# Optimization experiments

Measured on AMD Instinct MI355X. Metric: run time of the kernel, lower is better.

The kernel has to match this reference:

```python
import jax, jax.numpy as jnp
import numpy as np

EPS = 1e-5

def bn(x, g, b):
    # training-mode BatchNorm2d: normalize over all axes except channel axis 1
    ax = (0,) + tuple(range(2, x.ndim))
    m = x.mean(ax, keepdims=True)
    v = x.var(ax, keepdims=True)
    sh = (1, -1) + (1,) * (x.ndim - 2)
    return (x - m) * jax.lax.rsqrt(v + EPS) * g.reshape(sh) + b.reshape(sh)

def setup_inputs():
    key = jax.random.key(0)
    ks = jax.random.split(key, 7)
    N, C, H, W, G = 2, 128, 128, 128, 8
    gp = C // G  # group_planes = 16
    f32 = jnp.float32
    x = jax.random.normal(ks[0], (N, C, H, W), f32)
    wq = jax.random.normal(ks[1], (C // 2, C), f32) * np.float32(np.sqrt(1.0 / (C * gp)))
    wk = jax.random.normal(ks[2], (C // 2, C), f32) * np.float32(np.sqrt(1.0 / C))
    wv = jax.random.normal(ks[3], (C, C), f32) * np.float32(np.sqrt(1.0 / C))
    q_rel = jax.random.normal(ks[4], (gp // 2, 2 * H - 1), f32) * np.float32(np.sqrt(2.0 / C))
    k_rel = jax.random.normal(ks[5], (gp // 2, 2 * H - 1), f32) * np.float32(np.sqrt(2.0 / C))
    v_rel = jax.random.normal(ks[6], (gp, 2 * H - 1), f32) * np.float32(np.sqrt(1.0 / C))
    d = dict(x=x, wq=wq, wk=wk, wv=wv, q_rel=q_rel, k_rel=k_rel, v_rel=v_rel)
    for name, ch in [("bnq", C // 2), ("bnk", C // 2), ("bnv", C), ("bnqk", G), ("bnqr", G), ("bnkr", G), ("bnsv", C), ("bnsve", C)]:
        d[name + "_g"] = jnp.ones((ch,), f32)
        d[name + "_b"] = jnp.zeros((ch,), f32)
    return d

def reference(x, wq, wk, wv, q_rel, k_rel, v_rel, bnq_g, bnq_b, bnk_g, bnk_b, bnv_g, bnv_b, bnqk_g, bnqk_b, bnqr_g, bnqr_b, bnkr_g, bnkr_b, bnsv_g, bnsv_b, bnsve_g, bnsve_b):
    N, C, H, W = x.shape
    G = 8
    gp = C // G
    # 1x1 conv == channel matmul
    q = bn(jnp.einsum('oc,bchw->bohw', wq, x), bnq_g, bnq_b)
    k = bn(jnp.einsum('oc,bchw->bohw', wk, x), bnk_g, bnk_b)
    v = bn(jnp.einsum('oc,bchw->bohw', wv, x), bnv_g, bnv_b)
    # relative embedding gather: emb[c, j, i] = rel[c, j - i + H - 1]
    idx = jnp.arange(H)[:, None] - jnp.arange(H)[None, :] + (H - 1)  # [H, H]
    q_emb = q_rel[:, idx]
    k_emb = k_rel[:, idx]
    v_emb = v_rel[:, idx]
    qg = q.reshape(N, G, gp // 2, H, W)
    kg = k.reshape(N, G, gp // 2, H, W)
    vg = v.reshape(N, G, gp, H, W)
    qr = jnp.einsum('bgciw,cij->bgijw', qg, q_emb)
    qr = bn(qr.reshape(N, G, H * H, W), bnqr_g, bnqr_b).reshape(N, G, H, H, W)
    kr = jnp.einsum('bgciw,cij->bgijw', kg, k_emb)
    kr = bn(kr.reshape(N, G, H * H, W), bnkr_g, bnkr_b).reshape(N, G, H, H, W)
    kr = kr.transpose(0, 1, 3, 2, 4)
    qk = jnp.einsum('bgciw,bgcjw->bgijw', qg, kg)
    qk = bn(qk.reshape(N, G, H * H, W), bnqk_g, bnqk_b).reshape(N, G, H, H, W)
    sim = jax.nn.softmax(qk + qr + kr, axis=3)  # [N, G, H(i), H(j), W]
    sv = jnp.einsum('bgijw,bgcjw->bgciw', sim, vg).reshape(N, C, H, W)
    sve = jnp.einsum('bgijw,cji->bgciw', sim, v_emb).reshape(N, C, H, W)
    return bn(sv, bnsv_g, bnsv_b) + bn(sve, bnsve_g, bnsve_b)
```

## Files before the change

### kernel.cpp

```cpp
#include <hip/hip_runtime.h>
#include <hip/hip_fp16.h>


#define HW 16384

__device__ __forceinline__ float warp_sum(float v) {
#pragma unroll
  for (int o = 32; o > 0; o >>= 1) v += __shfl_down(v, o);
  return v;
}

__global__ __launch_bounds__(256) void k_transpose(const float* __restrict__ in, float* __restrict__ out) {
  __shared__ float t[32][33];
  int plane = blockIdx.y;
  int th = (blockIdx.x >> 2) * 32;
  int tw = (blockIdx.x & 3) * 32;
  const float* p = in + (size_t)plane * HW;
  float* q = out + (size_t)plane * HW;
  int lx = threadIdx.x, ly = threadIdx.y;
#pragma unroll
  for (int r = ly; r < 32; r += 8) t[r][lx] = p[(th + r) * 128 + tw + lx];
  __syncthreads();
#pragma unroll
  for (int r = ly; r < 32; r += 8) q[(tw + r) * 128 + th + lx] = t[lx][r];
}

__global__ __launch_bounds__(256) void k_wT(const float* __restrict__ wq, const float* __restrict__ wk,
                                            const float* __restrict__ wv, float* __restrict__ WT) {
  int idx = blockIdx.x * 256 + threadIdx.x;
  int och = idx & 255, c = idx >> 8;
  const float* wrow = och < 64 ? wq + och * 128 : (och < 128 ? wk + (och - 64) * 128 : wv + (och - 128) * 128);
  WT[c * 256 + och] = wrow[c];
}

__global__ __launch_bounds__(256) void k_qkv(const float* __restrict__ xT, const float* __restrict__ WT,
                                             float* __restrict__ qkvT) {
  __shared__ float Xs[64][64];
  __shared__ float Ws[64][64];
  int pb = blockIdx.x * 64;
  int ob = blockIdx.y * 64;
  int b = blockIdx.z;
  const float* xb = xT + (size_t)b * (128 * HW);
  int tid = threadIdx.x;
  int tx = tid & 15, ty = tid >> 4;
  float acc[4][4] = {};
  for (int ks = 0; ks < 2; ++ks) {
    for (int idx = tid; idx < 4096; idx += 256) {
      int c = idx >> 6, p = idx & 63;
      Xs[c][p] = xb[(ks * 64 + c) * HW + pb + p];
    }
    for (int idx = tid; idx < 4096; idx += 256) {
      int c = idx >> 6, o = idx & 63;
      Ws[c][o] = WT[(ks * 64 + c) * 256 + ob + o];
    }
    __syncthreads();
#pragma unroll 8
    for (int kk = 0; kk < 64; ++kk) {
      float a0 = Ws[kk][ty * 4 + 0], a1 = Ws[kk][ty * 4 + 1], a2 = Ws[kk][ty * 4 + 2], a3 = Ws[kk][ty * 4 + 3];
      float4 bv = *reinterpret_cast<const float4*>(&Xs[kk][tx * 4]);
      acc[0][0] += a0 * bv.x; acc[0][1] += a0 * bv.y; acc[0][2] += a0 * bv.z; acc[0][3] += a0 * bv.w;
      acc[1][0] += a1 * bv.x; acc[1][1] += a1 * bv.y; acc[1][2] += a1 * bv.z; acc[1][3] += a1 * bv.w;
      acc[2][0] += a2 * bv.x; acc[2][1] += a2 * bv.y; acc[2][2] += a2 * bv.z; acc[2][3] += a2 * bv.w;
      acc[3][0] += a3 * bv.x; acc[3][1] += a3 * bv.y; acc[3][2] += a3 * bv.z; acc[3][3] += a3 * bv.w;
    }
    __syncthreads();
  }
#pragma unroll
  for (int r = 0; r < 4; ++r) {
    int row = ob + ty * 4 + r;
    float4 o4 = make_float4(acc[r][0], acc[r][1], acc[r][2], acc[r][3]);
    *reinterpret_cast<float4*>(&qkvT[(size_t)(b * 256 + row) * HW + pb + tx * 4]) = o4;
  }
}

__global__ __launch_bounds__(256) void k_qkv_stats(const float* __restrict__ qkvT, double* __restrict__ statsQKV) {
  __shared__ float r1[4], r2[4];
  int ch = blockIdx.x;
  float s = 0.f, s2 = 0.f;
  for (int b = 0; b < 2; ++b) {
    const float* p = qkvT + (size_t)(b * 256 + ch) * HW;
    for (int idx = threadIdx.x; idx < HW; idx += 256) { float v = p[idx]; s += v; s2 += v * v; }
  }
  s = warp_sum(s); s2 = warp_sum(s2);
  int wid = threadIdx.x >> 6;
  if ((threadIdx.x & 63) == 0) { r1[wid] = s; r2[wid] = s2; }
  __syncthreads();
  if (threadIdx.x == 0) {
    statsQKV[2 * ch]     = (double)(r1[0] + r1[1] + r1[2] + r1[3]);
    statsQKV[2 * ch + 1] = (double)(r2[0] + r2[1] + r2[2] + r2[3]);
  }
}

__global__ __launch_bounds__(128) void k_rel_tables(const float* __restrict__ q_rel, const float* __restrict__ k_rel,
                                                    float* __restrict__ tabs) {
  int tbl = blockIdx.x / 44, item = blockIdx.x % 44;
  const float* rel = tbl ? k_rel : q_rel;
  float* out = tabs + tbl * 5632;
  int i = threadIdx.x;
  float s = 0.f;
  if (item < 8) {
    const float* r = rel + item * 255 + i;
    for (int d = 0; d < 128; ++d) s += r[d];
  } else {
    int p = item - 8;
    int pp = p, c = 0;
    while (pp >= 8 - c) { pp -= 8 - c; ++c; }
    int c2 = c + pp;
    const float* ra = rel + c * 255 + i;
    const float* rb = rel + c2 * 255 + i;
    for (int d = 0; d < 128; ++d) s += ra[d] * rb[d];
  }
  out[item * 128 + i] = s;
}

__global__ __launch_bounds__(128) void k_qkr_stats(
    const float* __restrict__ qkvT, const double* __restrict__ statsQKV,
    const float* __restrict__ bnq_g, const float* __restrict__ bnq_b,
    const float* __restrict__ bnk_g, const float* __restrict__ bnk_b,
    const float* __restrict__ tabs, double* __restrict__ statsA) {
  __shared__ float red[92][2];
  int slice = blockIdx.x;
  int w = slice & 127, g = (slice >> 7) & 7, b = slice >> 10;
  int i = threadIdx.x;
  float qn[8], kn[8];
  const float* qbase = qkvT + (size_t)(b * 256 + g * 8) * HW + w * 128 + i;
  const float* kbase = qkvT + (size_t)(b * 256 + 64 + g * 8) * HW + w * 128 + i;
#pragma unroll
  for (int c = 0; c < 8; ++c) {
    {
      int och = g * 8 + c;
      double su = statsQKV[2 * och], sq = statsQKV[2 * och + 1];
      double mu = su * (1.0 / 32768.0);
      float var = (float)(sq * (1.0 / 32768.0) - mu * mu);
      float sc = bnq_g[och] * rsqrtf(var + 1e-5f);
      qn[c] = qbase[c * HW] * sc + (bnq_b[och] - (float)mu * sc);
    }
    {
      int gi = g * 8 + c, och = 64 + gi;
      double su = statsQKV[2 * och], sq = statsQKV[2 * och + 1];
      double mu = su * (1.0 / 32768.0);
      float var = (float)(sq * (1.0 / 32768.0) - mu * mu);
      float sc = bnk_g[gi] * rsqrtf(var + 1e-5f);
      kn[c] = kbase[c * HW] * sc + (bnk_b[gi] - (float)mu * sc);
    }
  }
  float vals[92];
  int n = 0;
#pragma unroll
  for (int c = 0; c < 8; ++c) vals[n++] = qn[c];
#pragma unroll
  for (int c = 0; c < 8; ++c) vals[n++] = kn[c];
#pragma unroll
  for (int c = 0; c < 8; ++c)
#pragma unroll
    for (int c2 = c; c2 < 8; ++c2) vals[n++] = qn[c] * qn[c2];
#pragma unroll
  for (int c = 0; c < 8; ++c)
#pragma unroll
    for (int c2 = c; c2 < 8; ++c2) vals[n++] = kn[c] * kn[c2];
  float sqr = 0.f, s2qr = 0.f, skr = 0.f, s2kr = 0.f;
#pragma unroll
  for (int c = 0; c < 8; ++c) {
    sqr += qn[c] * tabs[c * 128 + i];
    skr += kn[c] * tabs[5632 + c * 128 + i];
  }
  {
    int p = 0;
#pragma unroll
    for (int c = 0; c < 8; ++c)
#pragma unroll
      for (int c2 = c; c2 < 8; ++c2) {
        float f = (c == c2) ? 1.f : 2.f;
        s2qr += f * qn[c] * qn[c2] * tabs[1024 + p * 128 + i];
        s2kr += f * kn[c] * kn[c2] * tabs[5632 + 1024 + p * 128 + i];
        ++p;
      }
  }
  vals[88] = sqr; vals[89] = s2qr; vals[90] = skr; vals[91] = s2kr;
  int lane = i & 63, wid = i >> 6;
#pragma unroll
  for (int vv = 0; vv < 92; ++vv) {
    float r = warp_sum(vals[vv]);
    if (lane == 0) red[vv][wid] = r;
  }
  __syncthreads();
  if (i == 0) {
    float f[92];
#pragma unroll
    for (int vv = 0; vv < 92; ++vv) f[vv] = red[vv][0] + red[vv][1];
    float sS = 0.f, s2S = 0.f;
#pragma unroll
    for (int c = 0; c < 8; ++c) sS += f[c] * f[8 + c];
    {
      int p = 0;
#pragma unroll
      for (int c = 0; c < 8; ++c)
#pragma unroll
        for (int c2 = c; c2 < 8; ++c2) { float fm = (c == c2) ? 1.f : 2.f; s2S += fm * f[16 + p] * f[52 + p]; ++p; }
    }
    atomicAdd(&statsA[(0 * 8 + g) * 2 + 0], (double)sS);
    atomicAdd(&statsA[(0 * 8 + g) * 2 + 1], (double)s2S);
    atomicAdd(&statsA[(1 * 8 + g) * 2 + 0], (double)f[88]);
    atomicAdd(&statsA[(1 * 8 + g) * 2 + 1], (double)f[89]);
    atomicAdd(&statsA[(2 * 8 + g) * 2 + 0], (double)f[90]);
    atomicAdd(&statsA[(2 * 8 + g) * 2 + 1], (double)f[91]);
  }
}

__global__ __launch_bounds__(256) void k_relT(const float* __restrict__ q_rel, const float* __restrict__ k_rel,
                                              float* __restrict__ relT) {
  int idx = blockIdx.x * 256 + threadIdx.x;
  if (idx < 2040) {
    int d = idx >> 3, c = idx & 7;
    relT[idx] = q_rel[c * 255 + d];
  } else if (idx < 4080) {
    int j = idx - 2040;
    int d = j >> 3, c = j & 7;
    relT[2040 + j] = k_rel[c * 255 + d];
  }
}

__global__ __launch_bounds__(256) void k_attn(
    const float* __restrict__ qkvT,
    const double* __restrict__ statsQKV, const double* __restrict__ statsA,
    const float* __restrict__ relTq, const float* __restrict__ relTk, const float* __restrict__ v_rel,
    const float* __restrict__ bnq_g, const float* __restrict__ bnq_b,
    const float* __restrict__ bnk_g, const float* __restrict__ bnk_b,
    const float* __restrict__ bnv_g, const float* __restrict__ bnv_b,
    const float* __restrict__ bnqk_g, const float* __restrict__ bnqk_b,
    const float* __restrict__ bnqr_g, const float* __restrict__ bnqr_b,
    const float* __restrict__ bnkr_g, const float* __restrict__ bnkr_b,
    float* __restrict__ svT, float* __restrict__ sveT) {
  __shared__ float Ks[128][8];
  __shared__ float Vs[128][16];
  __shared__ __half Wr[255 * 20];
  __shared__ float nsc[32], nsh[32];
  int slice = blockIdx.x;
  int w = slice & 127, g = (slice >> 7) & 7, b = slice >> 10;
  int tid = threadIdx.x;
  if (tid < 32) {
    int och, gi; const float* gm; const float* bt;
    if (tid < 8)       { gi = g * 8 + tid;        och = gi;       gm = bnq_g; bt = bnq_b; }
    else if (tid < 16) { gi = g * 8 + (tid - 8);  och = 64 + gi;  gm = bnk_g; bt = bnk_b; }
    else               { gi = g * 16 + (tid - 16); och = 128 + gi; gm = bnv_g; bt = bnv_b; }
    double su = statsQKV[2 * och], sq = statsQKV[2 * och + 1];
    double mu = su * (1.0 / 32768.0);
    float var = (float)(sq * (1.0 / 32768.0) - mu * mu);
    float sc = gm[gi] * rsqrtf(var + 1e-5f);
    nsc[tid] = sc;
    nsh[tid] = bt[gi] - (float)mu * sc;
  }
  __syncthreads();
  {
    const float* kbase = qkvT + (size_t)(b * 256 + 64 + g * 8) * HW + w * 128;
    for (int idx = tid; idx < 1024; idx += 256) {
      int c = idx >> 7, jj = idx & 127;
      Ks[jj][c] = kbase[c * HW + jj] * nsc[8 + c] + nsh[8 + c];
    }
    const float* vbase = qkvT + (size_t)(b * 256 + 128 + g * 16) * HW + w * 128;
    for (int idx = tid; idx < 2048; idx += 256) {
      int c = idx >> 7, jj = idx & 127;
      Vs[jj][c] = vbase[c * HW + jj] * nsc[16 + c] + nsh[16 + c];
    }
    for (int idx = tid; idx < 4096; idx += 256) {
      int c = idx >> 8, d = idx & 255;
      if (d < 255) Wr[d * 20 + c] = __float2half(v_rel[c * 255 + d]);
    }
  }
  int i = tid >> 1, h = tid & 1;
  float qreg[8];
  {
    const float* qbase = qkvT + (size_t)(b * 256 + g * 8) * HW + w * 128;
#pragma unroll
    for (int c = 0; c < 8; ++c) qreg[c] = qbase[c * HW + i] * nsc[c] + nsh[c];
  }
  float aS, aQR, aKR, offs;
  {
    const double inv = 1.0 / 4194304.0;
    double s0 = statsA[(0 * 8 + g) * 2], q0 = statsA[(0 * 8 + g) * 2 + 1];
    double s1 = statsA[(1 * 8 + g) * 2], q1 = statsA[(1 * 8 + g) * 2 + 1];
    double s2 = statsA[(2 * 8 + g) * 2], q2 = statsA[(2 * 8 + g) * 2 + 1];
    double m0 = s0 * inv, m1 = s1 * inv, m2 = s2 * inv;
    float v0 = (float)(q0 * inv - m0 * m0);
    float v1 = (float)(q1 * inv - m1 * m1);
    float v2 = (float)(q2 * inv - m2 * m2);
    aS  = bnqk_g[g] * rsqrtf(v0 + 1e-5f);
    aQR = bnqr_g[g] * rsqrtf(v1 + 1e-5f);
    aKR = bnkr_g[g] * rsqrtf(v2 + 1e-5f);
    offs = (bnqk_b[g] - (float)m0 * aS) + (bnqr_b[g] - (float)m1 * aQR) + (bnkr_b[g] - (float)m2 * aKR);
    offs -= 5.545177444479562f;
  }
  __syncthreads();

  const int jbase = h << 6;
  float l = 0.f;
  float asv[16] = {};
  __half2 hacc[8];
#pragma unroll
  for (int u = 0; u < 8; ++u) hacc[u] = __float2half2_rn(0.f);
  const float* qrp = relTq + (size_t)(127 + i - jbase) * 8;
  const float* krp = relTk + (size_t)(127 - i + jbase) * 8;
  const __half* wp = Wr + (127 - i + jbase) * 20;
  const float* kp  = &Ks[jbase][0];
  const float* vp  = &Vs[jbase][0];

#pragma unroll 2
  for (int jj = 0; jj < 64; ++jj) {
    float4 ka = *reinterpret_cast<const float4*>(kp);
    float4 kb = *reinterpret_cast<const float4*>(kp + 4);
    float4 qa = *reinterpret_cast<const float4*>(qrp);
    float4 qb = *reinterpret_cast<const float4*>(qrp + 4);
    float4 ra = *reinterpret_cast<const float4*>(krp);
    float4 rb = *reinterpret_cast<const float4*>(krp + 4);
    float S  = qreg[0] * ka.x + qreg[1] * ka.y + qreg[2] * ka.z + qreg[3] * ka.w
             + qreg[4] * kb.x + qreg[5] * kb.y + qreg[6] * kb.z + qreg[7] * kb.w;
    float QR = qreg[0] * qa.x + qreg[1] * qa.y + qreg[2] * qa.z + qreg[3] * qa.w
             + qreg[4] * qb.x + qreg[5] * qb.y + qreg[6] * qb.z + qreg[7] * qb.w;
    float KR = ka.x * ra.x + ka.y * ra.y + ka.z * ra.z + ka.w * ra.w
             + kb.x * rb.x + kb.y * rb.y + kb.z * rb.z + kb.w * rb.w;
    float a = fmaf(S, aS, fmaf(QR, aQR, fmaf(KR, aKR, offs)));
    float e = __expf(a);
    l += e;
    float4 v0 = *reinterpret_cast<const float4*>(vp);
    float4 v1 = *reinterpret_cast<const float4*>(vp + 4);
    float4 v2 = *reinterpret_cast<const float4*>(vp + 8);
    float4 v3 = *reinterpret_cast<const float4*>(vp + 12);
    asv[0]  += e * v0.x; asv[1]  += e * v0.y; asv[2]  += e * v0.z; asv[3]  += e * v0.w;
    asv[4]  += e * v1.x; asv[5]  += e * v1.y; asv[6]  += e * v1.z; asv[7]  += e * v1.w;
    asv[8]  += e * v2.x; asv[9]  += e * v2.y; asv[10] += e * v2.z; asv[11] += e * v2.w;
    asv[12] += e * v3.x; asv[13] += e * v3.y; asv[14] += e * v3.z; asv[15] += e * v3.w;
    __half2 eh2 = __float2half2_rn(e);
    float2 w0 = *reinterpret_cast<const float2*>(wp);
    float2 w1 = *reinterpret_cast<const float2*>(wp + 4);
    float2 w2 = *reinterpret_cast<const float2*>(wp + 8);
    float2 w3 = *reinterpret_cast<const float2*>(wp + 12);
    const __half2* h0 = reinterpret_cast<const __half2*>(&w0);
    const __half2* h1 = reinterpret_cast<const __half2*>(&w1);
    const __half2* h2 = reinterpret_cast<const __half2*>(&w2);
    const __half2* h3 = reinterpret_cast<const __half2*>(&w3);
    hacc[0] = __hfma2(eh2, h0[0], hacc[0]); hacc[1] = __hfma2(eh2, h0[1], hacc[1]);
    hacc[2] = __hfma2(eh2, h1[0], hacc[2]); hacc[3] = __hfma2(eh2, h1[1], hacc[3]);
    hacc[4] = __hfma2(eh2, h2[0], hacc[4]); hacc[5] = __hfma2(eh2, h2[1], hacc[5]);
    hacc[6] = __hfma2(eh2, h3[0], hacc[6]); hacc[7] = __hfma2(eh2, h3[1], hacc[7]);
    qrp -= 8; krp += 8; wp += 20; kp += 8; vp += 16;
  }
  float L = l + __shfl_xor(l, 1);
  float linv = 1.f / L;
  float* outp = (h ? sveT : svT) + (size_t)slice * 2048 + i;
#pragma unroll
  for (int c = 0; c < 16; ++c) {
    float vsv = asv[c] + __shfl_xor(asv[c], 1);
    float hv = (c & 1) ? __high2float(hacc[c >> 1]) : __low2float(hacc[c >> 1]);
    float vse = hv + __shfl_xor(hv, 1);
    outp[c * 128] = (h ? vse : vsv) * linv;
  }
}

__global__ __launch_bounds__(256) void k_sv_stats(const float* __restrict__ svT, const float* __restrict__ sveT,
                                                  double* __restrict__ statsSV) {
  __shared__ float r1[4], r2[4];
  int ch = blockIdx.x;
  const float* base = (ch < 128) ? svT : sveT;
  int c = ch & 127, g = c >> 4, cc = c & 15;
  float s = 0.f, s2 = 0.f;
  for (int idx = threadIdx.x; idx < 32768; idx += 256) {
    int bw = idx >> 7, ii = idx & 127;
    int bb = bw >> 7, wwi = bw & 127;
    float v = base[(size_t)(((bb * 8 + g) * 128) + wwi) * 2048 + cc * 128 + ii];
    s += v; s2 += v * v;
  }
  s = warp_sum(s); s2 = warp_sum(s2);
  int wid = threadIdx.x >> 6;
  if ((threadIdx.x & 63) == 0) { r1[wid] = s; r2[wid] = s2; }
  __syncthreads();
  if (threadIdx.x == 0) {
    statsSV[2 * ch]     = (double)(r1[0] + r1[1] + r1[2] + r1[3]);
    statsSV[2 * ch + 1] = (double)(r2[0] + r2[1] + r2[2] + r2[3]);
  }
}

__global__ __launch_bounds__(256) void k_final(const float* __restrict__ svT, const float* __restrict__ sveT,
                                               const double* __restrict__ statsSV,
                                               const float* __restrict__ bnsv_g, const float* __restrict__ bnsv_b,
                                               const float* __restrict__ bnsve_g, const float* __restrict__ bnsve_b,
                                               float* __restrict__ out) {
  __shared__ float t[32][33];
  int plane = blockIdx.y;
  int b = plane >> 7, c = plane & 127;
  int g = c >> 4, cc = c & 15;
  double s = statsSV[2 * c], s2 = statsSV[2 * c + 1];
  double mu1 = s * (1.0 / 32768.0);
  float var1 = (float)(s2 * (1.0 / 32768.0) - mu1 * mu1);
  float sc1 = bnsv_g[c] * rsqrtf(var1 + 1e-5f);
  float sh1 = bnsv_b[c] - (float)mu1 * sc1;
  double se = statsSV[2 * (128 + c)], se2 = statsSV[2 * (128 + c) + 1];
  double mu2 = se * (1.0 / 32768.0);
  float var2 = (float)(se2 * (1.0 / 32768.0) - mu2 * mu2);
  float sc2 = bnsve_g[c] * rsqrtf(var2 + 1e-5f);
  float sh2 = bnsve_b[c] - (float)mu2 * sc2;
  int tw = (blockIdx.x & 3) * 32, ti = (blockIdx.x >> 2) * 32;
  int lx = threadIdx.x, ly = threadIdx.y;
#pragma unroll
  for (int r = ly; r < 32; r += 8) {
    int wr = tw + r, ii = ti + lx;
    size_t off = (size_t)((b * 8 + g) * 128 + wr) * 2048 + cc * 128 + ii;
    t[r][lx] = svT[off] * sc1 + sh1 + sveT[off] * sc2 + sh2;
  }
  __syncthreads();
#pragma unroll
  for (int r = ly; r < 32; r += 8)
    out[(size_t)plane * HW + (ti + r) * 128 + tw + lx] = t[lx][r];
}

extern "C" void kernel_launch(void* const* d_in, const int* in_sizes, int n_in,
                              void* d_out, int out_size, void* d_ws, size_t ws_size,
                              hipStream_t stream) {
  const float* x      = (const float*)d_in[0];
  const float* wq     = (const float*)d_in[1];
  const float* wk     = (const float*)d_in[2];
  const float* wv     = (const float*)d_in[3];
  const float* q_rel  = (const float*)d_in[4];
  const float* k_rel  = (const float*)d_in[5];
  const float* v_rel  = (const float*)d_in[6];
  const float* bnq_g  = (const float*)d_in[7];
  const float* bnq_b  = (const float*)d_in[8];
  const float* bnk_g  = (const float*)d_in[9];
  const float* bnk_b  = (const float*)d_in[10];
  const float* bnv_g  = (const float*)d_in[11];
  const float* bnv_b  = (const float*)d_in[12];
  const float* bnqk_g = (const float*)d_in[13];
  const float* bnqk_b = (const float*)d_in[14];
  const float* bnqr_g = (const float*)d_in[15];
  const float* bnqr_b = (const float*)d_in[16];
  const float* bnkr_g = (const float*)d_in[17];
  const float* bnkr_b = (const float*)d_in[18];
  const float* bnsv_g = (const float*)d_in[19];
  const float* bnsv_b = (const float*)d_in[20];
  const float* bnsve_g = (const float*)d_in[21];
  const float* bnsve_b = (const float*)d_in[22];
  float* out = (float*)d_out;

  float* wsf  = (float*)d_ws;
  float* xT   = wsf;
  float* svT  = wsf;
  float* qkvT = wsf + 4194304;
  float* sveT = wsf + 12582912;
  float* tabs = wsf + 16777216;
  float* relTq = tabs;
  float* relTk = tabs + 2040;
  float* WT   = wsf + 16788480;
  double* statsQKV = (double*)(wsf + 16821248);
  double* statsA   = statsQKV + 512;
  double* statsSV  = statsA + 48;

  hipMemsetAsync(statsA, 0, 48 * sizeof(double), stream);
  k_transpose<<<dim3(16, 256), dim3(32, 8), 0, stream>>>(x, xT);
  k_wT<<<128, 256, 0, stream>>>(wq, wk, wv, WT);
  k_qkv<<<dim3(256, 4, 2), 256, 0, stream>>>(xT, WT, qkvT);
  k_qkv_stats<<<256, 256, 0, stream>>>(qkvT, statsQKV);
  k_rel_tables<<<88, 128, 0, stream>>>(q_rel, k_rel, tabs);
  k_qkr_stats<<<2048, 128, 0, stream>>>(qkvT, statsQKV, bnq_g, bnq_b, bnk_g, bnk_b, tabs, statsA);
  k_relT<<<16, 256, 0, stream>>>(q_rel, k_rel, relTq);
  k_attn<<<2048, 256, 0, stream>>>(qkvT, statsQKV, statsA, relTq, relTk, v_rel,
                                   bnq_g, bnq_b, bnk_g, bnk_b, bnv_g, bnv_b,
                                   bnqk_g, bnqk_b, bnqr_g, bnqr_b, bnkr_g, bnkr_b,
                                   svT, sveT);
  k_sv_stats<<<256, 256, 0, stream>>>(svT, sveT, statsSV);
  k_final<<<dim3(16, 256), dim3(32, 8), 0, stream>>>(svT, sveT, statsSV,
                                                     bnsv_g, bnsv_b, bnsve_g, bnsve_b, out);
  (void)in_sizes; (void)n_in; (void)out_size; (void)ws_size;
}
```

Baseline: 455.3 us.

## Process four w-slices per attention block, two query rows per thread

```diff
diff --git a/kernel.cpp b/kernel.cpp
--- a/kernel.cpp
+++ b/kernel.cpp
@@ -231,13 +231,13 @@
     const float* __restrict__ bnqr_g, const float* __restrict__ bnqr_b,
     const float* __restrict__ bnkr_g, const float* __restrict__ bnkr_b,
     float* __restrict__ svT, float* __restrict__ sveT) {
-  __shared__ float Ks[128][8];
-  __shared__ float Vs[128][16];
-  __shared__ __half Wr[255 * 20];
+  __shared__ float Ks[4][128][8];
+  __shared__ float Vs[4][128][16];
+  __shared__ __half Wh[2][255][8];
   __shared__ float nsc[32], nsh[32];
-  int slice = blockIdx.x;
-  int w = slice & 127, g = (slice >> 7) & 7, b = slice >> 10;
   int tid = threadIdx.x;
+  int slice0 = blockIdx.x * 4;
+  int w0 = slice0 & 127, g = (slice0 >> 7) & 7, b = slice0 >> 10;
   if (tid < 32) {
     int och, gi; const float* gm; const float* bt;
     if (tid < 8)       { gi = g * 8 + tid;        och = gi;       gm = bnq_g; bt = bnq_b; }
@@ -251,28 +251,17 @@
     nsh[tid] = bt[gi] - (float)mu * sc;
   }
   __syncthreads();
-  {
-    const float* kbase = qkvT + (size_t)(b * 256 + 64 + g * 8) * HW + w * 128;
-    for (int idx = tid; idx < 1024; idx += 256) {
-      int c = idx >> 7, jj = idx & 127;
-      Ks[jj][c] = kbase[c * HW + jj] * nsc[8 + c] + nsh[8 + c];
-    }
-    const float* vbase = qkvT + (size_t)(b * 256 + 128 + g * 16) * HW + w * 128;
-    for (int idx = tid; idx < 2048; idx += 256) {
-      int c = idx >> 7, jj = idx & 127;
-      Vs[jj][c] = vbase[c * HW + jj] * nsc[16 + c] + nsh[16 + c];
-    }
-    for (int idx = tid; idx < 4096; idx += 256) {
-      int c = idx >> 8, d = idx & 255;
-      if (d < 255) Wr[d * 20 + c] = __float2half(v_rel[c * 255 + d]);
-    }
-  }
-  int i = tid >> 1, h = tid & 1;
-  float qreg[8];
-  {
-    const float* qbase = qkvT + (size_t)(b * 256 + g * 8) * HW + w * 128;
-#pragma unroll
-    for (int c = 0; c < 8; ++c) qreg[c] = qbase[c * HW + i] * nsc[c] + nsh[c];
+  for (int idx = tid; idx < 4096; idx += 256) {
+    int j = idx & 127, c = (idx >> 7) & 7, s = idx >> 10;
+    Ks[s][j][c] = qkvT[(size_t)(b * 256 + 64 + g * 8 + c) * HW + (w0 + s) * 128 + j] * nsc[8 + c] + nsh[8 + c];
+  }
+  for (int idx = tid; idx < 8192; idx += 256) {
+    int j = idx & 127, c = (idx >> 7) & 15, s = idx >> 11;
+    Vs[s][j][c] = qkvT[(size_t)(b * 256 + 128 + g * 16 + c) * HW + (w0 + s) * 128 + j] * nsc[16 + c] + nsh[16 + c];
+  }
+  for (int idx = tid; idx < 4080; idx += 256) {
+    int c8 = idx / 2040, r = idx - c8 * 2040, d = r >> 3, e = r & 7;
+    Wh[c8][d][e] = __float2half(v_rel[(c8 * 8 + e) * 255 + d]);
   }
   float aS, aQR, aKR, offs;
   {
@@ -292,67 +281,102 @@
   }
   __syncthreads();
 
-  const int jbase = h << 6;
-  float l = 0.f;
-  float asv[16] = {};
-  __half2 hacc[8];
-#pragma unroll
-  for (int u = 0; u < 8; ++u) hacc[u] = __float2half2_rn(0.f);
-  const float* qrp = relTq + (size_t)(127 + i - jbase) * 8;
-  const float* krp = relTk + (size_t)(127 - i + jbase) * 8;
-  const __half* wp = Wr + (127 - i + jbase) * 20;
-  const float* kp  = &Ks[jbase][0];
-  const float* vp  = &Vs[jbase][0];
+  int wv = tid >> 6, lane = tid & 63;
+  int slice = slice0 + wv, w = w0 + wv;
+  int i0 = lane, i1 = lane + 64;
+  float q0r[8], q1r[8];
+  {
+    const float* qbase = qkvT + (size_t)(b * 256 + g * 8) * HW + w * 128;
+#pragma unroll
+    for (int c = 0; c < 8; ++c) {
+      q0r[c] = qbase[c * HW + i0] * nsc[c] + nsh[c];
+      q1r[c] = qbase[c * HW + i1] * nsc[c] + nsh[c];
+    }
+  }
+  float l0 = 0.f, l1 = 0.f;
+  float asv0[16] = {}, asv1[16] = {};
+  __half2 ha0[8], ha1[8];
+#pragma unroll
+  for (int u = 0; u < 8; ++u) { ha0[u] = __float2half2_rn(0.f); ha1[u] = __float2half2_rn(0.f); }
+  const float* Kp = &Ks[wv][0][0];
+  const float* Vp = &Vs[wv][0][0];
 
 #pragma unroll 2
-  for (int jj = 0; jj < 64; ++jj) {
-    float4 ka = *reinterpret_cast<const float4*>(kp);
-    float4 kb = *reinterpret_cast<const float4*>(kp + 4);
-    float4 qa = *reinterpret_cast<const float4*>(qrp);
-    float4 qb = *reinterpret_cast<const float4*>(qrp + 4);
-    float4 ra = *reinterpret_cast<const float4*>(krp);
-    float4 rb = *reinterpret_cast<const float4*>(krp + 4);
-    float S  = qreg[0] * ka.x + qreg[1] * ka.y + qreg[2] * ka.z + qreg[3] * ka.w
-             + qreg[4] * kb.x + qreg[5] * kb.y + qreg[6] * kb.z + qreg[7] * kb.w;
-    float QR = qreg[0] * qa.x + qreg[1] * qa.y + qreg[2] * qa.z + qreg[3] * qa.w
-             + qreg[4] * qb.x + qreg[5] * qb.y + qreg[6] * qb.z + qreg[7] * qb.w;
-    float KR = ka.x * ra.x + ka.y * ra.y + ka.z * ra.z + ka.w * ra.w
-             + kb.x * rb.x + kb.y * rb.y + kb.z * rb.z + kb.w * rb.w;
-    float a = fmaf(S, aS, fmaf(QR, aQR, fmaf(KR, aKR, offs)));
-    float e = __expf(a);
-    l += e;
-    float4 v0 = *reinterpret_cast<const float4*>(vp);
-    float4 v1 = *reinterpret_cast<const float4*>(vp + 4);
-    float4 v2 = *reinterpret_cast<const float4*>(vp + 8);
-    float4 v3 = *reinterpret_cast<const float4*>(vp + 12);
-    asv[0]  += e * v0.x; asv[1]  += e * v0.y; asv[2]  += e * v0.z; asv[3]  += e * v0.w;
-    asv[4]  += e * v1.x; asv[5]  += e * v1.y; asv[6]  += e * v1.z; asv[7]  += e * v1.w;
-    asv[8]  += e * v2.x; asv[9]  += e * v2.y; asv[10] += e * v2.z; asv[11] += e * v2.w;
-    asv[12] += e * v3.x; asv[13] += e * v3.y; asv[14] += e * v3.z; asv[15] += e * v3.w;
-    __half2 eh2 = __float2half2_rn(e);
-    float2 w0 = *reinterpret_cast<const float2*>(wp);
-    float2 w1 = *reinterpret_cast<const float2*>(wp + 4);
-    float2 w2 = *reinterpret_cast<const float2*>(wp + 8);
-    float2 w3 = *reinterpret_cast<const float2*>(wp + 12);
-    const __half2* h0 = reinterpret_cast<const __half2*>(&w0);
-    const __half2* h1 = reinterpret_cast<const __half2*>(&w1);
-    const __half2* h2 = reinterpret_cast<const __half2*>(&w2);
-    const __half2* h3 = reinterpret_cast<const __half2*>(&w3);
-    hacc[0] = __hfma2(eh2, h0[0], hacc[0]); hacc[1] = __hfma2(eh2, h0[1], hacc[1]);
-    hacc[2] = __hfma2(eh2, h1[0], hacc[2]); hacc[3] = __hfma2(eh2, h1[1], hacc[3]);
-    hacc[4] = __hfma2(eh2, h2[0], hacc[4]); hacc[5] = __hfma2(eh2, h2[1], hacc[5]);
-    hacc[6] = __hfma2(eh2, h3[0], hacc[6]); hacc[7] = __hfma2(eh2, h3[1], hacc[7]);
-    qrp -= 8; krp += 8; wp += 20; kp += 8; vp += 16;
-  }
-  float L = l + __shfl_xor(l, 1);
-  float linv = 1.f / L;
-  float* outp = (h ? sveT : svT) + (size_t)slice * 2048 + i;
+  for (int j = 0; j < 128; ++j) {
+    float4 ka = *reinterpret_cast<const float4*>(Kp + j * 8);
+    float4 kb = *reinterpret_cast<const float4*>(Kp + j * 8 + 4);
+    int dq = 127 + i0 - j;
+    int d0 = 127 - i0 + j;
+    const float4* qp0 = reinterpret_cast<const float4*>(relTq + dq * 8);
+    const float4* qp1 = reinterpret_cast<const float4*>(relTq + (dq + 64) * 8);
+    const float4* rp0 = reinterpret_cast<const float4*>(relTk + d0 * 8);
+    const float4* rp1 = reinterpret_cast<const float4*>(relTk + (d0 - 64) * 8);
+    float4 qa0 = qp0[0], qb0 = qp0[1], qa1 = qp1[0], qb1 = qp1[1];
+    float4 ra0 = rp0[0], rb0 = rp0[1], ra1 = rp1[0], rb1 = rp1[1];
+    float S0 = q0r[0]*ka.x + q0r[1]*ka.y + q0r[2]*ka.z + q0r[3]*ka.w
+             + q0r[4]*kb.x + q0r[5]*kb.y + q0r[6]*kb.z + q0r[7]*kb.w;
+    float S1 = q1r[0]*ka.x + q1r[1]*ka.y + q1r[2]*ka.z + q1r[3]*ka.w
+             + q1r[4]*kb.x + q1r[5]*kb.y + q1r[6]*kb.z + q1r[7]*kb.w;
+    float QR0 = q0r[0]*qa0.x + q0r[1]*qa0.y + q0r[2]*qa0.z + q0r[3]*qa0.w
+              + q0r[4]*qb0.x + q0r[5]*qb0.y + q0r[6]*qb0.z + q0r[7]*qb0.w;
+    float QR1 = q1r[0]*qa1.x + q1r[1]*qa1.y + q1r[2]*qa1.z + q1r[3]*qa1.w
+              + q1r[4]*qb1.x + q1r[5]*qb1.y + q1r[6]*qb1.z + q1r[7]*qb1.w;
+    float KR0 = ka.x*ra0.x + ka.y*ra0.y + ka.z*ra0.z + ka.w*ra0.w
+              + kb.x*rb0.x + kb.y*rb0.y + kb.z*rb0.z + kb.w*rb0.w;
+    float KR1 = ka.x*ra1.x + ka.y*ra1.y + ka.z*ra1.z + ka.w*ra1.w
+              + kb.x*rb1.x + kb.y*rb1.y + kb.z*rb1.z + kb.w*rb1.w;
+    float a0 = fmaf(S0, aS, fmaf(QR0, aQR, fmaf(KR0, aKR, offs)));
+    float a1 = fmaf(S1, aS, fmaf(QR1, aQR, fmaf(KR1, aKR, offs)));
+    float e0 = __expf(a0);
+    float e1 = __expf(a1);
+    l0 += e0; l1 += e1;
+    float4 v0 = *reinterpret_cast<const float4*>(Vp + j * 16);
+    float4 v1 = *reinterpret_cast<const float4*>(Vp + j * 16 + 4);
+    float4 v2 = *reinterpret_cast<const float4*>(Vp + j * 16 + 8);
+    float4 v3 = *reinterpret_cast<const float4*>(Vp + j * 16 + 12);
+    asv0[0]  += e0*v0.x; asv0[1]  += e0*v0.y; asv0[2]  += e0*v0.z; asv0[3]  += e0*v0.w;
+    asv0[4]  += e0*v1.x; asv0[5]  += e0*v1.y; asv0[6]  += e0*v1.z; asv0[7]  += e0*v1.w;
+    asv0[8]  += e0*v2.x; asv0[9]  += e0*v2.y; asv0[10] += e0*v2.z; asv0[11] += e0*v2.w;
+    asv0[12] += e0*v3.x; asv0[13] += e0*v3.y; asv0[14] += e0*v3.z; asv0[15] += e0*v3.w;
+    asv1[0]  += e1*v0.x; asv1[1]  += e1*v0.y; asv1[2]  += e1*v0.z; asv1[3]  += e1*v0.w;
+    asv1[4]  += e1*v1.x; asv1[5]  += e1*v1.y; asv1[6]  += e1*v1.z; asv1[7]  += e1*v1.w;
+    asv1[8]  += e1*v2.x; asv1[9]  += e1*v2.y; asv1[10] += e1*v2.z; asv1[11] += e1*v2.w;
+    asv1[12] += e1*v3.x; asv1[13] += e1*v3.y; asv1[14] += e1*v3.z; asv1[15] += e1*v3.w;
+    float4 wa0 = *reinterpret_cast<const float4*>(&Wh[0][d0][0]);
+    float4 wb0 = *reinterpret_cast<const float4*>(&Wh[1][d0][0]);
+    float4 wa1 = *reinterpret_cast<const float4*>(&Wh[0][d0 - 64][0]);
+    float4 wb1 = *reinterpret_cast<const float4*>(&Wh[1][d0 - 64][0]);
+    __half2 eh0 = __float2half2_rn(e0), eh1 = __float2half2_rn(e1);
+    {
+      const __half2* pa = reinterpret_cast<const __half2*>(&wa0);
+      const __half2* pb = reinterpret_cast<const __half2*>(&wb0);
+      ha0[0] = __hfma2(eh0, pa[0], ha0[0]); ha0[1] = __hfma2(eh0, pa[1], ha0[1]);
+      ha0[2] = __hfma2(eh0, pa[2], ha0[2]); ha0[3] = __hfma2(eh0, pa[3], ha0[3]);
+      ha0[4] = __hfma2(eh0, pb[0], ha0[4]); ha0[5] = __hfma2(eh0, pb[1], ha0[5]);
+      ha0[6] = __hfma2(eh0, pb[2], ha0[6]); ha0[7] = __hfma2(eh0, pb[3], ha0[7]);
+    }
+    {
+      const __half2* pa = reinterpret_cast<const __half2*>(&wa1);
+      const __half2* pb = reinterpret_cast<const __half2*>(&wb1);
+      ha1[0] = __hfma2(eh1, pa[0], ha1[0]); ha1[1] = __hfma2(eh1, pa[1], ha1[1]);
+      ha1[2] = __hfma2(eh1, pa[2], ha1[2]); ha1[3] = __hfma2(eh1, pa[3], ha1[3]);
+      ha1[4] = __hfma2(eh1, pb[0], ha1[4]); ha1[5] = __hfma2(eh1, pb[1], ha1[5]);
+      ha1[6] = __hfma2(eh1, pb[2], ha1[6]); ha1[7] = __hfma2(eh1, pb[3], ha1[7]);
+    }
+  }
+  float li0 = 1.f / l0, li1 = 1.f / l1;
+  float* osv0  = svT  + (size_t)slice * 2048 + i0;
+  float* osve0 = sveT + (size_t)slice * 2048 + i0;
+  float* osv1  = svT  + (size_t)slice * 2048 + i1;
+  float* osve1 = sveT + (size_t)slice * 2048 + i1;
 #pragma unroll
   for (int c = 0; c < 16; ++c) {
-    float vsv = asv[c] + __shfl_xor(asv[c], 1);
-    float hv = (c & 1) ? __high2float(hacc[c >> 1]) : __low2float(hacc[c >> 1]);
-    float vse = hv + __shfl_xor(hv, 1);
-    outp[c * 128] = (h ? vse : vsv) * linv;
+    float h0 = (c & 1) ? __high2float(ha0[c >> 1]) : __low2float(ha0[c >> 1]);
+    float h1 = (c & 1) ? __high2float(ha1[c >> 1]) : __low2float(ha1[c >> 1]);
+    osv0[c * 128]  = asv0[c] * li0;
+    osve0[c * 128] = h0 * li0;
+    osv1[c * 128]  = asv1[c] * li1;
+    osve1[c * 128] = h1 * li1;
   }
 }
 
@@ -461,10 +485,10 @@
   k_rel_tables<<<88, 128, 0, stream>>>(q_rel, k_rel, tabs);
   k_qkr_stats<<<2048, 128, 0, stream>>>(qkvT, statsQKV, bnq_g, bnq_b, bnk_g, bnk_b, tabs, statsA);
   k_relT<<<16, 256, 0, stream>>>(q_rel, k_rel, relTq);
-  k_attn<<<2048, 256, 0, stream>>>(qkvT, statsQKV, statsA, relTq, relTk, v_rel,
-                                   bnq_g, bnq_b, bnk_g, bnk_b, bnv_g, bnv_b,
-                                   bnqk_g, bnqk_b, bnqr_g, bnqr_b, bnkr_g, bnkr_b,
-                                   svT, sveT);
+  k_attn<<<512, 256, 0, stream>>>(qkvT, statsQKV, statsA, relTq, relTk, v_rel,
+                                  bnq_g, bnq_b, bnk_g, bnk_b, bnv_g, bnv_b,
+                                  bnqk_g, bnqk_b, bnqr_g, bnqr_b, bnkr_g, bnkr_b,
+                                  svT, sveT);
   k_sv_stats<<<256, 256, 0, stream>>>(svT, sveT, statsSV);
   k_final<<<dim3(16, 256), dim3(32, 8), 0, stream>>>(svT, sveT, statsSV,
                                                      bnsv_g, bnsv_b, bnsve_g, bnsve_b, out);
```

Result: faster. 414.2 us (-9.0%).
